# Kernel tuning notes

Hardware: AMD Instinct MI355X
Metric: run time of the kernel (lower is better)

The kernel has to match this reference:

```python
import jax, jax.numpy as jnp
import numpy as np

B, N, C, H, P = 8, 4096, 256, 4, 64  # batch, tokens, hidden, heads, proj_size


def setup_inputs() -> dict:
    key = jax.random.key(0)
    ks = jax.random.split(key, 6)
    sc = 0.02
    x = jax.random.normal(ks[0], (B, N, C), jnp.float32)
    bank = jax.random.normal(ks[1], (B, N, C), jnp.float32)  # unused by forward, kept for fidelity
    W_qkvv = jax.random.normal(ks[2], (4 * C, C), jnp.float32) * sc  # Linear(C, 4C), no bias
    W_E = jax.random.normal(ks[3], (P, N), jnp.float32) * sc          # E = F shared Linear(N, P)
    b_E = jnp.zeros((P,), jnp.float32)
    temperature = jnp.ones((H, 1, 1), jnp.float32)
    temperature2 = jnp.ones((H, 1, 1), jnp.float32)
    W_out1 = jax.random.normal(ks[4], (C // 2, C), jnp.float32) * sc  # out_proj (spatial branch)
    b_out1 = jnp.zeros((C // 2,), jnp.float32)
    W_out2 = jax.random.normal(ks[5], (C // 2, C), jnp.float32) * sc  # out_proj2 (channel branch)
    b_out2 = jnp.zeros((C // 2,), jnp.float32)
    prelu_a = jnp.array(0.25, jnp.float32)  # nn.PReLU() default: single shared slope
    return {"x": x, "bank": bank, "W_qkvv": W_qkvv, "W_E": W_E, "b_E": b_E,
            "temperature": temperature, "temperature2": temperature2,
            "W_out1": W_out1, "b_out1": b_out1, "W_out2": W_out2, "b_out2": b_out2,
            "prelu_a": prelu_a}


def _l2norm(t):
    # torch F.normalize(dim=-1): x / max(||x||_2, eps)
    return t / jnp.maximum(jnp.linalg.norm(t, axis=-1, keepdims=True), 1e-12)


def reference(x, bank, W_qkvv, W_E, b_E, temperature, temperature2,
              W_out1, b_out1, W_out2, b_out2, prelu_a):
    Bb, Nn, Cc = x.shape
    Hh = temperature.shape[0]
    d = Cc // Hh
    # qkvv projection -> [4, B, H, N, d], then transpose token/feature axes -> [B, H, d, N]
    qkvv = (x @ W_qkvv.T).reshape(Bb, Nn, 4, Hh, d).transpose(2, 0, 3, 1, 4)
    q, k, v_ca, v_sa = (qkvv[0].transpose(0, 1, 3, 2), qkvv[1].transpose(0, 1, 3, 2),
                        qkvv[2].transpose(0, 1, 3, 2), qkvv[3].transpose(0, 1, 3, 2))
    # shared linear E=F projects the token axis N -> P (applied to UNnormalized k, v_sa)
    k_proj = jnp.einsum('bhdn,pn->bhdp', k, W_E) + b_E      # [B,H,d,P]
    v_sa_proj = jnp.einsum('bhdn,pn->bhdp', v_sa, W_E) + b_E  # [B,H,d,P]
    qn = _l2norm(q)
    kn = _l2norm(k)
    # channel attention: [B,H,d,d]
    attn_ca = jax.nn.softmax(jnp.einsum('bhdn,bhen->bhde', qn, kn) * temperature, axis=-1)
    x_ca = jnp.einsum('bhde,bhen->bhdn', attn_ca, v_ca).transpose(0, 3, 1, 2).reshape(Bb, Nn, Cc)
    # spatial attention (projected): [B,H,N,P]
    attn_sa = jax.nn.softmax(jnp.einsum('bhdn,bhdp->bhnp', qn, k_proj) * temperature2, axis=-1)
    x_sa = jnp.einsum('bhnp,bhdp->bhnd', attn_sa, v_sa_proj).transpose(0, 2, 1, 3).reshape(Bb, Nn, Cc)
    x_sa = x_sa @ W_out1.T + b_out1
    x_ca = x_ca @ W_out2.T + b_out2
    out = jnp.concatenate([x_sa, x_ca], axis=-1)
    return jnp.where(out >= 0, out, prelu_a * out)  # PReLU
```

## Files before the change

kernel.cpp:

```cpp
#include <hip/hip_runtime.h>
#include <cstdint>
#include <cstddef>

constexpr int B_ = 8, N_ = 4096, C_ = 256, H_ = 4, D_ = 64, P_ = 64;
constexpr int OC_ = 4 * C_;
constexpr int M_  = B_ * N_;
constexpr int GX_ROWS = 320;
constexpr int KSPLIT_G = 8;

#define DEV_INLINE __device__ __forceinline__

typedef unsigned short ushort_t;
typedef __attribute__((ext_vector_type(8))) short short8;
typedef __attribute__((ext_vector_type(4))) short short4v;
typedef __attribute__((ext_vector_type(4))) float floatx4;

DEV_INLINE short f2bf(float f) {
  unsigned int u = __builtin_bit_cast(unsigned int, f);
  u += 0x7FFFu + ((u >> 16) & 1u);
  return (short)(u >> 16);
}
DEV_INLINE float bf2f(ushort_t u) {
  return __builtin_bit_cast(float, (unsigned int)u << 16);
}

constexpr size_t X4_  = (size_t)M_ * C_ / 4;
constexpr size_t WQ4_ = (size_t)OC_ * C_ / 4;
constexpr size_t W14_ = (size_t)128 * C_ / 4;
constexpr size_t WE4_ = (size_t)P_ * N_ / 4;
constexpr size_t TOT4_ = X4_ + WQ4_ + 2 * W14_ + WE4_;

__global__ __launch_bounds__(256) void k_cast(const float* __restrict__ x,
                                              const float* __restrict__ Wq,
                                              const float* __restrict__ W1,
                                              const float* __restrict__ W2,
                                              const float* __restrict__ WE,
                                              ushort_t* __restrict__ xb,
                                              ushort_t* __restrict__ wqb,
                                              ushort_t* __restrict__ w1b,
                                              ushort_t* __restrict__ w2b,
                                              ushort_t* __restrict__ web) {
  const size_t stride = (size_t)gridDim.x * 256;
  for (size_t i = blockIdx.x * 256 + threadIdx.x; i < TOT4_; i += stride) {
    const float* src;
    ushort_t* dst;
    size_t o;
    if (i < X4_) { src = x; dst = xb; o = i; }
    else if (i < X4_ + WQ4_) { src = Wq; dst = wqb; o = i - X4_; }
    else if (i < X4_ + WQ4_ + W14_) { src = W1; dst = w1b; o = i - X4_ - WQ4_; }
    else if (i < X4_ + WQ4_ + 2 * W14_) { src = W2; dst = w2b; o = i - X4_ - WQ4_ - W14_; }
    else { src = WE; dst = web; o = i - X4_ - WQ4_ - 2 * W14_; }
    float4 v = ((const float4*)src)[o];
    short4v s = {f2bf(v.x), f2bf(v.y), f2bf(v.z), f2bf(v.w)};
    *(short4v*)&dst[o * 4] = s;
  }
}

__global__ __launch_bounds__(256) void k_gram(const ushort_t* __restrict__ xb,
                                              const ushort_t* __restrict__ web,
                                              float* __restrict__ Gx) {
  __shared__ __align__(16) short As[128 * 64];
  __shared__ __align__(16) short Bs[128 * 64];
  const int job = blockIdx.x;
  const int ablk = job >> 1;
  const int bblk = job & 1;
  const int b = blockIdx.y >> 3;
  const int ksp = blockIdx.y & 7;
  const int t = threadIdx.x;
  const int lane = t & 63, wave = t >> 6;
  const int m16 = lane & 15, quad = lane >> 4;
  const int wm = (wave >> 1) << 6, wn = (wave & 1) << 6;
  floatx4 acc[4][4];
#pragma unroll
  for (int i = 0; i < 4; ++i)
#pragma unroll
    for (int j = 0; j < 4; ++j) acc[i][j] = (floatx4)(0.f);
  if (ablk == 2) {
#pragma unroll
    for (int i = 0; i < 8; ++i)
      *(unsigned int*)&As[64 * 64 + (i * 256 + t) * 2] = 0u;
  }
  const int c0 = (t & 31) * 4;
  const int tp = t >> 5;
#pragma unroll 1
  for (int it = 0; it < N_ / KSPLIT_G / 64; ++it) {
    const int n0 = ksp * (N_ / KSPLIT_G) + it * 64;
    __syncthreads();
#pragma unroll
    for (int q = 0; q < 4; ++q) {
      const int tok = q * 16 + 2 * tp;
      const size_t r0 = (size_t)(b * N_ + n0 + tok) * C_ + bblk * 128 + c0;
      short4v aa = *(const short4v*)&xb[r0];
      short4v cc = *(const short4v*)&xb[r0 + C_];
#pragma unroll
      for (int i = 0; i < 4; ++i) {
        const int r = c0 + i;
        const int col = tok ^ (8 * ((r >> 3) & 7));
        unsigned int w = (unsigned int)(ushort_t)aa[i] |
                         ((unsigned int)(ushort_t)cc[i] << 16);
        *(unsigned int*)&Bs[r * 64 + col] = w;
      }
    }
    if (ablk < 2) {
#pragma unroll
      for (int q = 0; q < 4; ++q) {
        const int tok = q * 16 + 2 * tp;
        const size_t r0 = (size_t)(b * N_ + n0 + tok) * C_ + ablk * 128 + c0;
        short4v aa = *(const short4v*)&xb[r0];
        short4v cc = *(const short4v*)&xb[r0 + C_];
#pragma unroll
        for (int i = 0; i < 4; ++i) {
          const int r = c0 + i;
          const int col = tok ^ (8 * ((r >> 3) & 7));
          unsigned int w = (unsigned int)(ushort_t)aa[i] |
                           ((unsigned int)(ushort_t)cc[i] << 16);
          *(unsigned int*)&As[r * 64 + col] = w;
        }
      }
    } else {
      const int oc8 = (t & 7) * 8;
      const int p0 = t >> 3;
#pragma unroll
      for (int q = 0; q < 2; ++q) {
        const int p = p0 + 32 * q;
        short8 v = *(const short8*)&web[(size_t)p * N_ + n0 + oc8];
        *(short8*)&As[p * 64 + (oc8 ^ (8 * ((p >> 3) & 7)))] = v;
      }
    }
    __syncthreads();
#pragma unroll
    for (int ks = 0; ks < 2; ++ks) {
      const int boct = ks * 32 + quad * 8;
      short8 af[4], bf[4];
#pragma unroll
      for (int i = 0; i < 4; ++i) {
        const int rA = wm + i * 16 + m16;
        af[i] = *(const short8*)&As[rA * 64 + (boct ^ (8 * ((rA >> 3) & 7)))];
      }
#pragma unroll
      for (int j = 0; j < 4; ++j) {
        const int rB = wn + j * 16 + m16;
        bf[j] = *(const short8*)&Bs[rB * 64 + (boct ^ (8 * ((rB >> 3) & 7)))];
      }
#pragma unroll
      for (int i = 0; i < 4; ++i)
#pragma unroll
        for (int j = 0; j < 4; ++j)
          acc[i][j] = __builtin_amdgcn_mfma_f32_16x16x32_bf16(af[i], bf[j], acc[i][j], 0, 0, 0);
    }
  }
#pragma unroll
  for (int i = 0; i < 4; ++i)
#pragma unroll
    for (int r = 0; r < 4; ++r) {
      const int rib = wm + i * 16 + quad * 4 + r;
      if (ablk == 2 && rib >= 64) continue;
      const size_t rowoff =
          ((size_t)b * GX_ROWS + ablk * 128 + rib) * 256 + bblk * 128 + wn;
#pragma unroll
      for (int j = 0; j < 4; ++j)
        atomicAdd(&Gx[rowoff + 16 * j + m16], acc[i][j][r]);
    }
}

__global__ __launch_bounds__(256) void k_gcast(const float* __restrict__ Gx,
                                               ushort_t* __restrict__ Gxb) {
  const int i = blockIdx.x * 256 + threadIdx.x;
  float4 v = ((const float4*)Gx)[i];
  short4v s = {f2bf(v.x), f2bf(v.y), f2bf(v.z), f2bf(v.w)};
  *(short4v*)&Gxb[i * 4] = s;
}

__global__ __launch_bounds__(256) void k_qv_mfma(const ushort_t* __restrict__ xb,
                                                 const ushort_t* __restrict__ wqb,
                                                 ushort_t* __restrict__ qv) {
  __shared__ __align__(16) short As[128 * 72];
  __shared__ __align__(16) short Bs[128 * 72];
  const int bm = blockIdx.x * 128;
  const int bo = blockIdx.y * 128;
  const int wrow_base = bo < 256 ? bo : bo + 256;
  const int t = threadIdx.x;
  const int oc = t & 7;
  const int rr = t >> 3;
  const int lane = t & 63, wave = t >> 6;
  const int m16 = lane & 15, quad = lane >> 4;
  const int wm = (wave >> 1) << 6, wn = (wave & 1) << 6;
  floatx4 acc[4][4];
#pragma unroll
  for (int i = 0; i < 4; ++i)
#pragma unroll
    for (int j = 0; j < 4; ++j) acc[i][j] = (floatx4)(0.f);
#pragma unroll 1
  for (int k0 = 0; k0 < 256; k0 += 64) {
    short8 a8[4], b8[4];
#pragma unroll
    for (int j = 0; j < 4; ++j) {
      const int r = rr + 32 * j;
      a8[j] = *(const short8*)&xb[(size_t)(bm + r) * 256 + k0 + 8 * oc];
      b8[j] = *(const short8*)&wqb[(size_t)(wrow_base + r) * 256 + k0 + 8 * oc];
    }
    __syncthreads();
#pragma unroll
    for (int j = 0; j < 4; ++j) {
      const int r = rr + 32 * j;
      *(short8*)&As[r * 72 + 8 * oc] = a8[j];
      *(short8*)&Bs[r * 72 + 8 * oc] = b8[j];
    }
    __syncthreads();
#pragma unroll
    for (int ks = 0; ks < 2; ++ks) {
      short8 af[4], bf[4];
#pragma unroll
      for (int i = 0; i < 4; ++i)
        af[i] = *(const short8*)&As[(wm + i * 16 + m16) * 72 + ks * 32 + quad * 8];
#pragma unroll
      for (int j = 0; j < 4; ++j)
        bf[j] = *(const short8*)&Bs[(wn + j * 16 + m16) * 72 + ks * 32 + quad * 8];
#pragma unroll
      for (int i = 0; i < 4; ++i)
#pragma unroll
        for (int j = 0; j < 4; ++j)
          acc[i][j] = __builtin_amdgcn_mfma_f32_16x16x32_bf16(af[i], bf[j], acc[i][j], 0, 0, 0);
    }
  }
#pragma unroll
  for (int i = 0; i < 4; ++i)
#pragma unroll
    for (int r = 0; r < 4; ++r) {
      const int gr = bm + wm + i * 16 + quad * 4 + r;
#pragma unroll
      for (int j = 0; j < 4; ++j)
        qv[(size_t)gr * 512 + bo + wn + j * 16 + m16] = (ushort_t)f2bf(acc[i][j][r]);
    }
}

__global__ __launch_bounds__(256) void k_t2gemm(const ushort_t* __restrict__ wqb,
                                                const ushort_t* __restrict__ Gxb,
                                                ushort_t* __restrict__ T2b) {
  __shared__ __align__(16) short As[128 * 72];
  __shared__ __align__(16) short Bs[128 * 72];
  const int bm = blockIdx.x * 128;
  const int b  = blockIdx.y >> 1;
  const int jb = blockIdx.y & 1;
  const int t = threadIdx.x;
  const int oc = t & 7;
  const int rr = t >> 3;
  const int lane = t & 63, wave = t >> 6;
  const int m16 = lane & 15, quad = lane >> 4;
  const int wm = (wave >> 1) << 6, wn = (wave & 1) << 6;
  const ushort_t* Bsrc = Gxb + ((size_t)b * GX_ROWS + jb * 128) * 256;
  floatx4 acc[4][4];
#pragma unroll
  for (int i = 0; i < 4; ++i)
#pragma unroll
    for (int j = 0; j < 4; ++j) acc[i][j] = (floatx4)(0.f);
#pragma unroll 1
  for (int k0 = 0; k0 < 256; k0 += 64) {
    short8 a8[4], b8[4];
#pragma unroll
    for (int j = 0; j < 4; ++j) {
      const int r = rr + 32 * j;
      a8[j] = *(const short8*)&wqb[(size_t)(bm + r) * 256 + k0 + 8 * oc];
      b8[j] = *(const short8*)&Bsrc[(size_t)r * 256 + k0 + 8 * oc];
    }
    __syncthreads();
#pragma unroll
    for (int j = 0; j < 4; ++j) {
      const int r = rr + 32 * j;
      *(short8*)&As[r * 72 + 8 * oc] = a8[j];
      *(short8*)&Bs[r * 72 + 8 * oc] = b8[j];
    }
    __syncthreads();
#pragma unroll
    for (int ks = 0; ks < 2; ++ks) {
      short8 af[4], bf[4];
#pragma unroll
      for (int i = 0; i < 4; ++i)
        af[i] = *(const short8*)&As[(wm + i * 16 + m16) * 72 + ks * 32 + quad * 8];
#pragma unroll
      for (int j = 0; j < 4; ++j)
        bf[j] = *(const short8*)&Bs[(wn + j * 16 + m16) * 72 + ks * 32 + quad * 8];
#pragma unroll
      for (int i = 0; i < 4; ++i)
#pragma unroll
        for (int j = 0; j < 4; ++j)
          acc[i][j] = __builtin_amdgcn_mfma_f32_16x16x32_bf16(af[i], bf[j], acc[i][j], 0, 0, 0);
    }
  }
#pragma unroll
  for (int i = 0; i < 4; ++i)
#pragma unroll
    for (int r = 0; r < 4; ++r) {
      const int gr = bm + wm + i * 16 + quad * 4 + r;
#pragma unroll
      for (int j = 0; j < 4; ++j)
        T2b[((size_t)b * 512 + gr) * 256 + jb * 128 + wn + j * 16 + m16] =
            (ushort_t)f2bf(acc[i][j][r]);
    }
}

__global__ __launch_bounds__(256) void k_rn(const ushort_t* __restrict__ wqb,
                                            const ushort_t* __restrict__ T2b,
                                            float* __restrict__ rn) {
  const int row_g = blockIdx.x * 4 + (threadIdx.x >> 6);
  const int lane = threadIdx.x & 63;
  const int b = row_g >> 9, row = row_g & 511;
  const short4v w  = *(const short4v*)&wqb[(size_t)row * 256 + lane * 4];
  const short4v tv = *(const short4v*)&T2b[((size_t)b * 512 + row) * 256 + lane * 4];
  float s = 0.f;
#pragma unroll
  for (int i = 0; i < 4; ++i) s += bf2f((ushort_t)w[i]) * bf2f((ushort_t)tv[i]);
#pragma unroll
  for (int o = 32; o; o >>= 1) s += __shfl_xor(s, o);
  if (lane == 0) rn[row_g] = 1.f / fmaxf(sqrtf(s), 1e-12f);
}

__global__ __launch_bounds__(64) void k_small(const ushort_t* __restrict__ wqb,
                                              const ushort_t* __restrict__ T2b,
                                              const ushort_t* __restrict__ Gxb,
                                              const float* __restrict__ bE,
                                              const float* __restrict__ rn,
                                              const float* __restrict__ t2,
                                              float* __restrict__ Sqk,
                                              ushort_t* __restrict__ ksb,
                                              ushort_t* __restrict__ vsb) {
  const int bh = blockIdx.x;
  const int job = blockIdx.y;
  const int b = bh >> 2, h = bh & 3;
  const int lane = threadIdx.x & 63;
  const int m16 = lane & 15, quad = lane >> 4;
  const int Abase = (job == 0 ? 0 : (job == 1 ? 256 : 768)) + h * 64;
  const ushort_t* Bp = (job == 0)
      ? T2b + ((size_t)b * 512 + 256 + h * 64) * 256
      : Gxb + ((size_t)b * GX_ROWS + 256) * 256;
  floatx4 acc[4][4];
#pragma unroll
  for (int i = 0; i < 4; ++i)
#pragma unroll
    for (int j = 0; j < 4; ++j) acc[i][j] = (floatx4)(0.f);
#pragma unroll
  for (int ks = 0; ks < 8; ++ks) {
    const int boct = ks * 32 + quad * 8;
    short8 af[4], bf[4];
#pragma unroll
    for (int i = 0; i < 4; ++i)
      af[i] = *(const short8*)&wqb[(size_t)(Abase + 16 * i + m16) * 256 + boct];
#pragma unroll
    for (int j = 0; j < 4; ++j)
      bf[j] = *(const short8*)&Bp[(size_t)(16 * j + m16) * 256 + boct];
#pragma unroll
    for (int i = 0; i < 4; ++i)
#pragma unroll
      for (int j = 0; j < 4; ++j)
        acc[i][j] = __builtin_amdgcn_mfma_f32_16x16x32_bf16(af[i], bf[j], acc[i][j], 0, 0, 0);
  }
  if (job == 0) {
#pragma unroll
    for (int i = 0; i < 4; ++i)
#pragma unroll
      for (int r = 0; r < 4; ++r) {
        const int d = 16 * i + quad * 4 + r;
#pragma unroll
        for (int j = 0; j < 4; ++j)
          Sqk[(size_t)bh * 4096 + d * 64 + 16 * j + m16] = acc[i][j][r];
      }
  } else if (job == 1) {
    const float tt = t2[h];
#pragma unroll
    for (int i = 0; i < 4; ++i)
#pragma unroll
      for (int r = 0; r < 4; ++r) {
        const int d = 16 * i + quad * 4 + r;
        const float rq = rn[b * 512 + h * 64 + d];
#pragma unroll
        for (int j = 0; j < 4; ++j) {
          const int p = 16 * j + m16;
          ksb[(size_t)bh * 4096 + p * 64 + d] =
              (ushort_t)f2bf((acc[i][j][r] + bE[p]) * rq * tt);
        }
      }
  } else {
#pragma unroll
    for (int i = 0; i < 4; ++i)
#pragma unroll
      for (int r = 0; r < 4; ++r) {
        const int d = 16 * i + quad * 4 + r;
#pragma unroll
        for (int j = 0; j < 4; ++j) {
          const int p = 16 * j + m16;
          vsb[(size_t)bh * 4096 + d * 64 + p] = (ushort_t)f2bf(acc[i][j][r] + bE[p]);
        }
      }
  }
}

__global__ __launch_bounds__(256) void k_ca_softmax(const float* __restrict__ Sqk,
                                                    const float* __restrict__ rn,
                                                    const float* __restrict__ temp,
                                                    ushort_t* __restrict__ ab) {
  const int w = threadIdx.x >> 6;
  const int lane = threadIdx.x & 63;
  const int row = blockIdx.x * 4 + w;
  const int b = row >> 8;
  const int rem = row & 255;
  const int h = rem >> 6;
  const float rq = rn[b * 512 + rem];
  const float rk = rn[b * 512 + 256 + h * 64 + lane];
  float l = Sqk[(size_t)row * 64 + lane] * rq * rk * temp[h];
  float m = l;
#pragma unroll
  for (int o = 32; o; o >>= 1) m = fmaxf(m, __shfl_xor(m, o));
  const float e = __expf(l - m);
  float s = e;
#pragma unroll
  for (int o = 32; o; o >>= 1) s += __shfl_xor(s, o);
  ab[(size_t)row * 64 + lane] = (ushort_t)f2bf(e / s);
}

__global__ __launch_bounds__(256) void k_ca_mfma(const ushort_t* __restrict__ qv,
                                                 const ushort_t* __restrict__ ab,
                                                 ushort_t* __restrict__ x_ca) {
  const int bh = blockIdx.x;
  const int b = bh >> 2, h = bh & 3;
  const int n0 = blockIdx.y * 128;
  const int lane = threadIdx.x & 63, wave = threadIdx.x >> 6;
  const int m16 = lane & 15, quad = lane >> 4;
  const ushort_t* abb = ab + (size_t)bh * 4096;
  short8 bf[2][4];
#pragma unroll
  for (int ks = 0; ks < 2; ++ks)
#pragma unroll
    for (int j = 0; j < 4; ++j)
      bf[ks][j] = *(const short8*)&abb[(16 * j + m16) * 64 + ks * 32 + quad * 8];
#pragma unroll
  for (int mm = 0; mm < 2; ++mm) {
    const int tokbase = n0 + 64 * mm + 16 * wave;
    const ushort_t* vrow =
        qv + (size_t)(b * N_ + tokbase + m16) * 512 + 256 + h * 64 + quad * 8;
    short8 af0 = *(const short8*)&vrow[0];
    short8 af1 = *(const short8*)&vrow[32];
    floatx4 o[4];
#pragma unroll
    for (int j = 0; j < 4; ++j) o[j] = (floatx4)(0.f);
#pragma unroll
    for (int j = 0; j < 4; ++j) {
      o[j] = __builtin_amdgcn_mfma_f32_16x16x32_bf16(af0, bf[0][j], o[j], 0, 0, 0);
      o[j] = __builtin_amdgcn_mfma_f32_16x16x32_bf16(af1, bf[1][j], o[j], 0, 0, 0);
    }
#pragma unroll
    for (int j = 0; j < 4; ++j)
#pragma unroll
      for (int r = 0; r < 4; ++r)
        x_ca[(size_t)(b * N_ + tokbase + quad * 4 + r) * C_ + h * 64 + 16 * j + m16] =
            (ushort_t)f2bf(o[j][r]);
  }
}

__global__ __launch_bounds__(256) void k_sa_mfma(const ushort_t* __restrict__ qv,
                                                 const ushort_t* __restrict__ ksb,
                                                 const ushort_t* __restrict__ vsb,
                                                 ushort_t* __restrict__ x_sa) {
  __shared__ float Pl[64][68];
  const int bh = blockIdx.x;
  const int b = bh >> 2, h = bh & 3;
  const int n0 = blockIdx.y * 64;
  const int lane = threadIdx.x & 63, wave = threadIdx.x >> 6;
  const int m16 = lane & 15, quad = lane >> 4;
  const ushort_t* qrow =
      qv + (size_t)(b * N_ + n0 + 16 * wave + m16) * 512 + h * 64 + quad * 8;
  short8 qf0 = *(const short8*)&qrow[0];
  short8 qf1 = *(const short8*)&qrow[32];
  const ushort_t* kb = ksb + (size_t)bh * 4096;
  const ushort_t* vb = vsb + (size_t)bh * 4096;
  short8 kf[2][4], vf[2][4];
#pragma unroll
  for (int ks = 0; ks < 2; ++ks)
#pragma unroll
    for (int j = 0; j < 4; ++j) {
      kf[ks][j] = *(const short8*)&kb[(16 * j + m16) * 64 + ks * 32 + quad * 8];
      vf[ks][j] = *(const short8*)&vb[(16 * j + m16) * 64 + ks * 32 + quad * 8];
    }
  floatx4 s[4];
#pragma unroll
  for (int j = 0; j < 4; ++j) s[j] = (floatx4)(0.f);
#pragma unroll
  for (int j = 0; j < 4; ++j) {
    s[j] = __builtin_amdgcn_mfma_f32_16x16x32_bf16(qf0, kf[0][j], s[j], 0, 0, 0);
    s[j] = __builtin_amdgcn_mfma_f32_16x16x32_bf16(qf1, kf[1][j], s[j], 0, 0, 0);
  }
  float p[4][4];
#pragma unroll
  for (int r = 0; r < 4; ++r) {
    float mr = fmaxf(fmaxf(s[0][r], s[1][r]), fmaxf(s[2][r], s[3][r]));
    mr = fmaxf(mr, __shfl_xor(mr, 1));
    mr = fmaxf(mr, __shfl_xor(mr, 2));
    mr = fmaxf(mr, __shfl_xor(mr, 4));
    mr = fmaxf(mr, __shfl_xor(mr, 8));
    float sr = 0.f;
#pragma unroll
    for (int j = 0; j < 4; ++j) {
      const float e = __expf(s[j][r] - mr);
      p[j][r] = e;
      sr += e;
    }
    sr += __shfl_xor(sr, 1);
    sr += __shfl_xor(sr, 2);
    sr += __shfl_xor(sr, 4);
    sr += __shfl_xor(sr, 8);
    const float inv = 1.f / sr;
#pragma unroll
    for (int j = 0; j < 4; ++j) p[j][r] *= inv;
  }
#pragma unroll
  for (int j = 0; j < 4; ++j)
#pragma unroll
    for (int r = 0; r < 4; ++r)
      Pl[16 * wave + quad * 4 + r][16 * j + m16] = p[j][r];
  __syncthreads();
  short8 pf[2];
#pragma unroll
// ... 67 lines not shown
#pragma unroll
    for (int ks = 0; ks < 2; ++ks) {
      short8 af[4], bf[4];
#pragma unroll
      for (int i = 0; i < 4; ++i)
        af[i] = *(const short8*)&As[(wm + i * 16 + m16) * 72 + ks * 32 + quad * 8];
#pragma unroll
      for (int j = 0; j < 4; ++j)
        bf[j] = *(const short8*)&Bs[(wn + j * 16 + m16) * 72 + ks * 32 + quad * 8];
#pragma unroll
      for (int i = 0; i < 4; ++i)
#pragma unroll
        for (int j = 0; j < 4; ++j)
          acc[i][j] = __builtin_amdgcn_mfma_f32_16x16x32_bf16(af[i], bf[j], acc[i][j], 0, 0, 0);
    }
  }
  const float slope = pa[0];
  float bj[4];
#pragma unroll
  for (int j = 0; j < 4; ++j) bj[j] = bias[wn + j * 16 + m16];
#pragma unroll
  for (int i = 0; i < 4; ++i)
#pragma unroll
    for (int r = 0; r < 4; ++r) {
      const int gr = bm + wm + i * 16 + quad * 4 + r;
#pragma unroll
      for (int j = 0; j < 4; ++j) {
        float v = acc[i][j][r] + bj[j];
        v = v >= 0.f ? v : slope * v;
        out[(size_t)gr * C_ + half * 128 + wn + j * 16 + m16] = v;
      }
    }
}

extern "C" void kernel_launch(void* const* d_in, const int* in_sizes, int n_in,
                              void* d_out, int out_size, void* d_ws, size_t ws_size,
                              hipStream_t stream) {
  (void)in_sizes; (void)n_in; (void)out_size; (void)ws_size;
  const float* x  = (const float*)d_in[0];
  const float* Wq = (const float*)d_in[2];
  const float* WE = (const float*)d_in[3];
  const float* bE = (const float*)d_in[4];
  const float* t1 = (const float*)d_in[5];
  const float* t2 = (const float*)d_in[6];
  const float* W1 = (const float*)d_in[7];
  const float* b1 = (const float*)d_in[8];
  const float* W2 = (const float*)d_in[9];
  const float* b2 = (const float*)d_in[10];
  const float* pa = (const float*)d_in[11];
  float* out = (float*)d_out;

  float* ws = (float*)d_ws;
  size_t off = 0;
  float* Sqk = ws + off; off += (size_t)32 * 4096;
  float* rn  = ws + off; off += (size_t)B_ * 512;
  float* Gx  = ws + off; off += (size_t)B_ * GX_ROWS * 256;
  ushort_t* qv  = (ushort_t*)(ws + off); off += (size_t)M_ * 512 / 2;
  ushort_t* xsa = (ushort_t*)(ws + off); off += (size_t)M_ * C_ / 2;
  ushort_t* xca = (ushort_t*)(ws + off); off += (size_t)M_ * C_ / 2;
  ushort_t* ksb = (ushort_t*)(ws + off); off += 32 * 4096 / 2;
  ushort_t* vsb = (ushort_t*)(ws + off); off += 32 * 4096 / 2;
  ushort_t* ab  = (ushort_t*)(ws + off); off += 32 * 4096 / 2;
  ushort_t* xb  = (ushort_t*)(ws + off); off += (size_t)M_ * C_ / 2;
  ushort_t* wqb = (ushort_t*)(ws + off); off += (size_t)OC_ * C_ / 2;
  ushort_t* w1b = (ushort_t*)(ws + off); off += (size_t)128 * C_ / 2;
  ushort_t* w2b = (ushort_t*)(ws + off); off += (size_t)128 * C_ / 2;
  ushort_t* web = (ushort_t*)(ws + off); off += (size_t)P_ * N_ / 2;
  ushort_t* Gxb = (ushort_t*)(ws + off); off += (size_t)B_ * GX_ROWS * 256 / 2;
  ushort_t* T2b = (ushort_t*)(ws + off); off += (size_t)B_ * 512 * 256 / 2;

  hipMemsetAsync(Gx, 0, (size_t)B_ * GX_ROWS * 256 * sizeof(float), stream);

  k_cast<<<2048, 256, 0, stream>>>(x, Wq, W1, W2, WE, xb, wqb, w1b, w2b, web);
  k_gram<<<dim3(6, B_ * KSPLIT_G), 256, 0, stream>>>(xb, web, Gx);
  k_qv_mfma<<<dim3(M_ / 128, 4), 256, 0, stream>>>(xb, wqb, qv);
  k_gcast<<<640, 256, 0, stream>>>(Gx, Gxb);
  k_t2gemm<<<dim3(4, B_ * 2), 256, 0, stream>>>(wqb, Gxb, T2b);
  k_rn<<<1024, 256, 0, stream>>>(wqb, T2b, rn);
  k_small<<<dim3(32, 3), 64, 0, stream>>>(wqb, T2b, Gxb, bE, rn, t2, Sqk, ksb, vsb);
  k_ca_softmax<<<512, 256, 0, stream>>>(Sqk, rn, t1, ab);
  k_ca_mfma<<<dim3(32, 32), 256, 0, stream>>>(qv, ab, xca);
  k_sa_mfma<<<dim3(32, 64), 256, 0, stream>>>(qv, ksb, vsb, xsa);
  k_out_mfma<<<dim3(M_ / 128, 2), 256, 0, stream>>>(xsa, xca, w1b, b1, w2b, b2, pa, out);
}
```

Baseline: 234.4 us.

## Fuse cast, QV GEMM, gram, norms and softmax into fewer kernel launches

Folds the fp32-to-bf16 cast of x into the QV projection GEMM, which now runs with 512-thread blocks and also writes xb. A side slice of that grid casts the weights. The gram kernel loads each x tile once for all column blocks and doubles the split-K factor. The separate Gx cast, norm and softmax kernels are folded into the mid kernels, and the channel and spatial attention kernels are merged into one launch. The aim is to cut kernel launches and intermediate global round-trips. In exchange, the fused kernels carry more branching and register pressure, and the larger split-K adds more atomics.

Result: slower. 255.8 us (+9.1%).

```diff
diff --git a/kernel.cpp b/kernel.cpp
--- a/kernel.cpp
+++ b/kernel.cpp
@@ -6,7 +6,7 @@
 constexpr int OC_ = 4 * C_;
 constexpr int M_  = B_ * N_;
 constexpr int GX_ROWS = 320;
-constexpr int KSPLIT_G = 8;
+constexpr int KSPLIT_G = 16;
 
 #define DEV_INLINE __device__ __forceinline__
 
@@ -23,220 +23,217 @@
 DEV_INLINE float bf2f(ushort_t u) {
   return __builtin_bit_cast(float, (unsigned int)u << 16);
 }
-
-constexpr size_t X4_  = (size_t)M_ * C_ / 4;
-constexpr size_t WQ4_ = (size_t)OC_ * C_ / 4;
-constexpr size_t W14_ = (size_t)128 * C_ / 4;
-constexpr size_t WE4_ = (size_t)P_ * N_ / 4;
-constexpr size_t TOT4_ = X4_ + WQ4_ + 2 * W14_ + WE4_;
-
-__global__ __launch_bounds__(256) void k_cast(const float* __restrict__ x,
-                                              const float* __restrict__ Wq,
-                                              const float* __restrict__ W1,
-                                              const float* __restrict__ W2,
-                                              const float* __restrict__ WE,
-                                              ushort_t* __restrict__ xb,
-                                              ushort_t* __restrict__ wqb,
-                                              ushort_t* __restrict__ w1b,
-                                              ushort_t* __restrict__ w2b,
-                                              ushort_t* __restrict__ web) {
-  const size_t stride = (size_t)gridDim.x * 256;
-  for (size_t i = blockIdx.x * 256 + threadIdx.x; i < TOT4_; i += stride) {
-    const float* src;
-    ushort_t* dst;
-    size_t o;
-    if (i < X4_) { src = x; dst = xb; o = i; }
-    else if (i < X4_ + WQ4_) { src = Wq; dst = wqb; o = i - X4_; }
-    else if (i < X4_ + WQ4_ + W14_) { src = W1; dst = w1b; o = i - X4_ - WQ4_; }
-    else if (i < X4_ + WQ4_ + 2 * W14_) { src = W2; dst = w2b; o = i - X4_ - WQ4_ - W14_; }
-    else { src = WE; dst = web; o = i - X4_ - WQ4_ - 2 * W14_; }
-    float4 v = ((const float4*)src)[o];
-    short4v s = {f2bf(v.x), f2bf(v.y), f2bf(v.z), f2bf(v.w)};
-    *(short4v*)&dst[o * 4] = s;
-  }
-}
-
-__global__ __launch_bounds__(256) void k_gram(const ushort_t* __restrict__ xb,
+DEV_INLINE short4v cvt4(float4 v) {
+  short4v s = {f2bf(v.x), f2bf(v.y), f2bf(v.z), f2bf(v.w)};
+  return s;
+}
+
+__global__ __launch_bounds__(512) void k_qv(const float* __restrict__ x,
+                                            const float* __restrict__ Wq,
+                                            const float* __restrict__ WE,
+                                            const float* __restrict__ W1,
+                                            const float* __restrict__ W2,
+                                            ushort_t* __restrict__ xb,
+                                            ushort_t* __restrict__ wqb,
+                                            ushort_t* __restrict__ web,
+                                            ushort_t* __restrict__ w1b,
+                                            ushort_t* __restrict__ w2b,
+                                            ushort_t* __restrict__ qv) {
+  __shared__ __align__(16) short As[128 * 72];
+  __shared__ __align__(16) short Bs[256 * 72];
+  const int cs = blockIdx.y;
+  const int t = threadIdx.x;
+  if (cs == 2) {
+    constexpr size_t WQ4 = 65536, WE4 = 65536, W14 = 8192;
+    constexpr size_t TOTW4 = WQ4 + WE4 + 2 * W14;
+    for (size_t i = (size_t)blockIdx.x * 512 + t; i < TOTW4; i += (size_t)256 * 512) {
+      const float* src; ushort_t* dst; size_t o;
+      if (i < WQ4) { src = Wq; dst = wqb; o = i; }
+      else if (i < WQ4 + WE4) { src = WE; dst = web; o = i - WQ4; }
+      else if (i < WQ4 + WE4 + W14) { src = W1; dst = w1b; o = i - WQ4 - WE4; }
+      else { src = W2; dst = w2b; o = i - WQ4 - WE4 - W14; }
+      float4 v = ((const float4*)src)[o];
+      *(short4v*)&dst[o * 4] = cvt4(v);
+    }
+    return;
+  }
+  const int bm = blockIdx.x * 128;
+  const int wbase = cs ? 512 : 0;
+  const int c = (t & 15) * 4;
+  const int row = t >> 4;
+  const int lane = t & 63, wave = t >> 6;
+  const int m16 = lane & 15, quad = lane >> 4;
+  const int wm = (wave >> 2) << 6, wn = (wave & 3) << 6;
+  floatx4 acc[4][4];
+#pragma unroll
+  for (int i = 0; i < 4; ++i)
+#pragma unroll
+    for (int j = 0; j < 4; ++j) acc[i][j] = (floatx4)(0.f);
+#pragma unroll 1
+  for (int k0 = 0; k0 < 256; k0 += 64) {
+    float4 av[4], bv[8];
+#pragma unroll
+    for (int rep = 0; rep < 4; ++rep)
+      av[rep] = *(const float4*)&x[(size_t)(bm + row + 32 * rep) * 256 + k0 + c];
+#pragma unroll
+    for (int rep = 0; rep < 8; ++rep)
+      bv[rep] = *(const float4*)&Wq[(size_t)(wbase + row + 32 * rep) * 256 + k0 + c];
+    __syncthreads();
+#pragma unroll
+    for (int rep = 0; rep < 4; ++rep) {
+      short4v s = cvt4(av[rep]);
+      *(short4v*)&As[(row + 32 * rep) * 72 + c] = s;
+      if (cs == 0)
+        *(short4v*)&xb[(size_t)(bm + row + 32 * rep) * 256 + k0 + c] = s;
+    }
+#pragma unroll
+    for (int rep = 0; rep < 8; ++rep)
+      *(short4v*)&Bs[(row + 32 * rep) * 72 + c] = cvt4(bv[rep]);
+    __syncthreads();
+#pragma unroll
+    for (int ks = 0; ks < 2; ++ks) {
+      short8 af[4], bf[4];
+#pragma unroll
+      for (int i = 0; i < 4; ++i)
+        af[i] = *(const short8*)&As[(wm + i * 16 + m16) * 72 + ks * 32 + quad * 8];
+#pragma unroll
+      for (int j = 0; j < 4; ++j)
+        bf[j] = *(const short8*)&Bs[(wn + j * 16 + m16) * 72 + ks * 32 + quad * 8];
+#pragma unroll
+      for (int i = 0; i < 4; ++i)
+#pragma unroll
+        for (int j = 0; j < 4; ++j)
+          acc[i][j] = __builtin_amdgcn_mfma_f32_16x16x32_bf16(af[i], bf[j], acc[i][j], 0, 0, 0);
+    }
+  }
+#pragma unroll
+  for (int i = 0; i < 4; ++i)
+#pragma unroll
+    for (int r = 0; r < 4; ++r) {
+      const int gr = bm + wm + i * 16 + quad * 4 + r;
+#pragma unroll
+      for (int j = 0; j < 4; ++j)
+        qv[(size_t)gr * 512 + cs * 256 + wn + j * 16 + m16] =
+            (ushort_t)f2bf(acc[i][j][r]);
+    }
+}
+
+__global__ __launch_bounds__(512) void k_gram(const ushort_t* __restrict__ xb,
                                               const ushort_t* __restrict__ web,
                                               float* __restrict__ Gx) {
-  __shared__ __align__(16) short As[128 * 64];
-  __shared__ __align__(16) short Bs[128 * 64];
+  __shared__ __align__(16) short Bs[256 * 64];
+  __shared__ __align__(16) short Ws[64 * 64];
   const int job = blockIdx.x;
-  const int ablk = job >> 1;
-  const int bblk = job & 1;
-  const int b = blockIdx.y >> 3;
-  const int ksp = blockIdx.y & 7;
+  const int b = blockIdx.y >> 4;
+  const int ksp = blockIdx.y & 15;
   const int t = threadIdx.x;
   const int lane = t & 63, wave = t >> 6;
   const int m16 = lane & 15, quad = lane >> 4;
-  const int wm = (wave >> 1) << 6, wn = (wave & 1) << 6;
+  const int wm = (wave >> 2) << 6;
+  const int wn4 = (wave & 3) << 6;
+  const int wn2 = wave << 5;
+  const int c0 = (t & 63) * 4;
+  const int tp = t >> 6;
   floatx4 acc[4][4];
 #pragma unroll
   for (int i = 0; i < 4; ++i)
 #pragma unroll
     for (int j = 0; j < 4; ++j) acc[i][j] = (floatx4)(0.f);
-  if (ablk == 2) {
-#pragma unroll
-    for (int i = 0; i < 8; ++i)
-      *(unsigned int*)&As[64 * 64 + (i * 256 + t) * 2] = 0u;
-  }
-  const int c0 = (t & 31) * 4;
-  const int tp = t >> 5;
 #pragma unroll 1
-  for (int it = 0; it < N_ / KSPLIT_G / 64; ++it) {
+  for (int it = 0; it < 4; ++it) {
     const int n0 = ksp * (N_ / KSPLIT_G) + it * 64;
     __syncthreads();
 #pragma unroll
     for (int q = 0; q < 4; ++q) {
       const int tok = q * 16 + 2 * tp;
-      const size_t r0 = (size_t)(b * N_ + n0 + tok) * C_ + bblk * 128 + c0;
+      const size_t r0 = (size_t)(b * N_ + n0 + tok) * C_ + c0;
       short4v aa = *(const short4v*)&xb[r0];
       short4v cc = *(const short4v*)&xb[r0 + C_];
 #pragma unroll
-      for (int i = 0; i < 4; ++i) {
-        const int r = c0 + i;
+      for (int ii = 0; ii < 4; ++ii) {
+        const int r = c0 + ii;
         const int col = tok ^ (8 * ((r >> 3) & 7));
-        unsigned int w = (unsigned int)(ushort_t)aa[i] |
-                         ((unsigned int)(ushort_t)cc[i] << 16);
+        unsigned int w = (unsigned int)(ushort_t)aa[ii] |
+                         ((unsigned int)(ushort_t)cc[ii] << 16);
         *(unsigned int*)&Bs[r * 64 + col] = w;
       }
     }
-    if (ablk < 2) {
-#pragma unroll
-      for (int q = 0; q < 4; ++q) {
-        const int tok = q * 16 + 2 * tp;
-        const size_t r0 = (size_t)(b * N_ + n0 + tok) * C_ + ablk * 128 + c0;
-        short4v aa = *(const short4v*)&xb[r0];
-        short4v cc = *(const short4v*)&xb[r0 + C_];
-#pragma unroll
-        for (int i = 0; i < 4; ++i) {
-          const int r = c0 + i;
-          const int col = tok ^ (8 * ((r >> 3) & 7));
-          unsigned int w = (unsigned int)(ushort_t)aa[i] |
-                           ((unsigned int)(ushort_t)cc[i] << 16);
-          *(unsigned int*)&As[r * 64 + col] = w;
-        }
-      }
-    } else {
+    if (job == 2) {
       const int oc8 = (t & 7) * 8;
       const int p0 = t >> 3;
-#pragma unroll
-      for (int q = 0; q < 2; ++q) {
-        const int p = p0 + 32 * q;
-        short8 v = *(const short8*)&web[(size_t)p * N_ + n0 + oc8];
-        *(short8*)&As[p * 64 + (oc8 ^ (8 * ((p >> 3) & 7)))] = v;
-      }
+      short8 v = *(const short8*)&web[(size_t)p0 * N_ + n0 + oc8];
+      *(short8*)&Ws[p0 * 64 + (oc8 ^ (8 * ((p0 >> 3) & 7)))] = v;
     }
     __syncthreads();
 #pragma unroll
     for (int ks = 0; ks < 2; ++ks) {
       const int boct = ks * 32 + quad * 8;
-      short8 af[4], bf[4];
-#pragma unroll
-      for (int i = 0; i < 4; ++i) {
-        const int rA = wm + i * 16 + m16;
-        af[i] = *(const short8*)&As[rA * 64 + (boct ^ (8 * ((rA >> 3) & 7)))];
-      }
-#pragma unroll
-      for (int j = 0; j < 4; ++j) {
-        const int rB = wn + j * 16 + m16;
-        bf[j] = *(const short8*)&Bs[rB * 64 + (boct ^ (8 * ((rB >> 3) & 7)))];
-      }
-#pragma unroll
-      for (int i = 0; i < 4; ++i)
+      if (job < 2) {
+        short8 af[4], bf[4];
+#pragma unroll
+        for (int i = 0; i < 4; ++i) {
+          const int rA = job * 128 + wm + 16 * i + m16;
+          af[i] = *(const short8*)&Bs[rA * 64 + (boct ^ (8 * ((rA >> 3) & 7)))];
+        }
+#pragma unroll
+        for (int j = 0; j < 4; ++j) {
+          const int rB = wn4 + 16 * j + m16;
+          bf[j] = *(const short8*)&Bs[rB * 64 + (boct ^ (8 * ((rB >> 3) & 7)))];
+        }
+#pragma unroll
+        for (int i = 0; i < 4; ++i)
+#pragma unroll
+          for (int j = 0; j < 4; ++j)
+            acc[i][j] = __builtin_amdgcn_mfma_f32_16x16x32_bf16(af[i], bf[j], acc[i][j], 0, 0, 0);
+      } else {
+        short8 af[4], bf[2];
+#pragma unroll
+        for (int i = 0; i < 4; ++i) {
+          const int rA = 16 * i + m16;
+          af[i] = *(const short8*)&Ws[rA * 64 + (boct ^ (8 * ((rA >> 3) & 7)))];
+        }
+#pragma unroll
+        for (int j = 0; j < 2; ++j) {
+          const int rB = wn2 + 16 * j + m16;
+          bf[j] = *(const short8*)&Bs[rB * 64 + (boct ^ (8 * ((rB >> 3) & 7)))];
+        }
+#pragma unroll
+        for (int i = 0; i < 4; ++i)
+#pragma unroll
+          for (int j = 0; j < 2; ++j)
+            acc[i][j] = __builtin_amdgcn_mfma_f32_16x16x32_bf16(af[i], bf[j], acc[i][j], 0, 0, 0);
+      }
+    }
+  }
+  if (job < 2) {
+#pragma unroll
+    for (int i = 0; i < 4; ++i)
+#pragma unroll
+      for (int r = 0; r < 4; ++r) {
+        const int grow = job * 128 + wm + 16 * i + quad * 4 + r;
+        const size_t rowoff = ((size_t)b * GX_ROWS + grow) * 256;
 #pragma unroll
         for (int j = 0; j < 4; ++j)
-          acc[i][j] = __builtin_amdgcn_mfma_f32_16x16x32_bf16(af[i], bf[j], acc[i][j], 0, 0, 0);
-    }
-  }
-#pragma unroll
-  for (int i = 0; i < 4; ++i)
-#pragma unroll
-    for (int r = 0; r < 4; ++r) {
-      const int rib = wm + i * 16 + quad * 4 + r;
-      if (ablk == 2 && rib >= 64) continue;
-      const size_t rowoff =
-          ((size_t)b * GX_ROWS + ablk * 128 + rib) * 256 + bblk * 128 + wn;
-#pragma unroll
-      for (int j = 0; j < 4; ++j)
-        atomicAdd(&Gx[rowoff + 16 * j + m16], acc[i][j][r]);
-    }
-}
-
-__global__ __launch_bounds__(256) void k_gcast(const float* __restrict__ Gx,
-                                               ushort_t* __restrict__ Gxb) {
-  const int i = blockIdx.x * 256 + threadIdx.x;
-  float4 v = ((const float4*)Gx)[i];
-  short4v s = {f2bf(v.x), f2bf(v.y), f2bf(v.z), f2bf(v.w)};
-  *(short4v*)&Gxb[i * 4] = s;
-}
-
-__global__ __launch_bounds__(256) void k_qv_mfma(const ushort_t* __restrict__ xb,
-                                                 const ushort_t* __restrict__ wqb,
-                                                 ushort_t* __restrict__ qv) {
-  __shared__ __align__(16) short As[128 * 72];
-  __shared__ __align__(16) short Bs[128 * 72];
-  const int bm = blockIdx.x * 128;
-  const int bo = blockIdx.y * 128;
-  const int wrow_base = bo < 256 ? bo : bo + 256;
-  const int t = threadIdx.x;
-  const int oc = t & 7;
-  const int rr = t >> 3;
-  const int lane = t & 63, wave = t >> 6;
-  const int m16 = lane & 15, quad = lane >> 4;
-  const int wm = (wave >> 1) << 6, wn = (wave & 1) << 6;
-  floatx4 acc[4][4];
-#pragma unroll
-  for (int i = 0; i < 4; ++i)
-#pragma unroll
-    for (int j = 0; j < 4; ++j) acc[i][j] = (floatx4)(0.f);
-#pragma unroll 1
-  for (int k0 = 0; k0 < 256; k0 += 64) {
-    short8 a8[4], b8[4];
-#pragma unroll
-    for (int j = 0; j < 4; ++j) {
-      const int r = rr + 32 * j;
-      a8[j] = *(const short8*)&xb[(size_t)(bm + r) * 256 + k0 + 8 * oc];
-      b8[j] = *(const short8*)&wqb[(size_t)(wrow_base + r) * 256 + k0 + 8 * oc];
-    }
-    __syncthreads();
-#pragma unroll
-    for (int j = 0; j < 4; ++j) {
-      const int r = rr + 32 * j;
-      *(short8*)&As[r * 72 + 8 * oc] = a8[j];
-      *(short8*)&Bs[r * 72 + 8 * oc] = b8[j];
-    }
-    __syncthreads();
-#pragma unroll
-    for (int ks = 0; ks < 2; ++ks) {
-      short8 af[4], bf[4];
-#pragma unroll
-      for (int i = 0; i < 4; ++i)
-        af[i] = *(const short8*)&As[(wm + i * 16 + m16) * 72 + ks * 32 + quad * 8];
-#pragma unroll
-      for (int j = 0; j < 4; ++j)
-        bf[j] = *(const short8*)&Bs[(wn + j * 16 + m16) * 72 + ks * 32 + quad * 8];
-#pragma unroll
-      for (int i = 0; i < 4; ++i)
-#pragma unroll
-        for (int j = 0; j < 4; ++j)
-          acc[i][j] = __builtin_amdgcn_mfma_f32_16x16x32_bf16(af[i], bf[j], acc[i][j], 0, 0, 0);
-    }
-  }
-#pragma unroll
-  for (int i = 0; i < 4; ++i)
-#pragma unroll
-    for (int r = 0; r < 4; ++r) {
-      const int gr = bm + wm + i * 16 + quad * 4 + r;
-#pragma unroll
-      for (int j = 0; j < 4; ++j)
-        qv[(size_t)gr * 512 + bo + wn + j * 16 + m16] = (ushort_t)f2bf(acc[i][j][r]);
-    }
-}
-
-__global__ __launch_bounds__(256) void k_t2gemm(const ushort_t* __restrict__ wqb,
-                                                const ushort_t* __restrict__ Gxb,
-                                                ushort_t* __restrict__ T2b) {
+          atomicAdd(&Gx[rowoff + wn4 + 16 * j + m16], acc[i][j][r]);
+      }
+  } else {
+#pragma unroll
+    for (int i = 0; i < 4; ++i)
+#pragma unroll
+      for (int r = 0; r < 4; ++r) {
+        const int grow = 256 + 16 * i + quad * 4 + r;
+        const size_t rowoff = ((size_t)b * GX_ROWS + grow) * 256;
+#pragma unroll
+        for (int j = 0; j < 2; ++j)
+          atomicAdd(&Gx[rowoff + wn2 + 16 * j + m16], acc[i][j][r]);
+      }
+  }
+}
+
+__global__ __launch_bounds__(256) void k_mid1(const ushort_t* __restrict__ wqb,
+                                              const float* __restrict__ Gx,
+                                              ushort_t* __restrict__ T2b,
+                                              float* __restrict__ ssq) {
   __shared__ __align__(16) short As[128 * 72];
   __shared__ __align__(16) short Bs[128 * 72];
   const int bm = blockIdx.x * 128;
@@ -248,7 +245,7 @@
   const int lane = t & 63, wave = t >> 6;
   const int m16 = lane & 15, quad = lane >> 4;
   const int wm = (wave >> 1) << 6, wn = (wave & 1) << 6;
-  const ushort_t* Bsrc = Gxb + ((size_t)b * GX_ROWS + jb * 128) * 256;
+  const float* Bsrc = Gx + ((size_t)b * GX_ROWS + jb * 128) * 256;
   floatx4 acc[4][4];
 #pragma unroll
   for (int i = 0; i < 4; ++i)
@@ -261,7 +258,12 @@
     for (int j = 0; j < 4; ++j) {
       const int r = rr + 32 * j;
       a8[j] = *(const short8*)&wqb[(size_t)(bm + r) * 256 + k0 + 8 * oc];
-      b8[j] = *(const short8*)&Bsrc[(size_t)r * 256 + k0 + 8 * oc];
+      float4 g0 = *(const float4*)&Bsrc[(size_t)r * 256 + k0 + 8 * oc];
+      float4 g1 = *(const float4*)&Bsrc[(size_t)r * 256 + k0 + 8 * oc + 4];
+      short8 bb;
+      bb[0] = f2bf(g0.x); bb[1] = f2bf(g0.y); bb[2] = f2bf(g0.z); bb[3] = f2bf(g0.w);
+      bb[4] = f2bf(g1.x); bb[5] = f2bf(g1.y); bb[6] = f2bf(g1.z); bb[7] = f2bf(g1.w);
+      b8[j] = bb;
     }
     __syncthreads();
 #pragma unroll
@@ -292,47 +294,37 @@
 #pragma unroll
     for (int r = 0; r < 4; ++r) {
       const int gr = bm + wm + i * 16 + quad * 4 + r;
-#pragma unroll
-      for (int j = 0; j < 4; ++j)
-        T2b[((size_t)b * 512 + gr) * 256 + jb * 128 + wn + j * 16 + m16] =
-            (ushort_t)f2bf(acc[i][j][r]);
-    }
-}
-
-__global__ __launch_bounds__(256) void k_rn(const ushort_t* __restrict__ wqb,
-                                            const ushort_t* __restrict__ T2b,
-                                            float* __restrict__ rn) {
-  const int row_g = blockIdx.x * 4 + (threadIdx.x >> 6);
-  const int lane = threadIdx.x & 63;
-  const int b = row_g >> 9, row = row_g & 511;
-  const short4v w  = *(const short4v*)&wqb[(size_t)row * 256 + lane * 4];
-  const short4v tv = *(const short4v*)&T2b[((size_t)b * 512 + row) * 256 + lane * 4];
-  float s = 0.f;
-#pragma unroll
-  for (int i = 0; i < 4; ++i) s += bf2f((ushort_t)w[i]) * bf2f((ushort_t)tv[i]);
-#pragma unroll
-  for (int o = 32; o; o >>= 1) s += __shfl_xor(s, o);
-  if (lane == 0) rn[row_g] = 1.f / fmaxf(sqrtf(s), 1e-12f);
-}
-
-__global__ __launch_bounds__(64) void k_small(const ushort_t* __restrict__ wqb,
-                                              const ushort_t* __restrict__ T2b,
-                                              const ushort_t* __restrict__ Gxb,
-                                              const float* __restrict__ bE,
-                                              const float* __restrict__ rn,
-                                              const float* __restrict__ t2,
-                                              float* __restrict__ Sqk,
-                                              ushort_t* __restrict__ ksb,
-                                              ushort_t* __restrict__ vsb) {
+      float s = 0.f;
+#pragma unroll
+      for (int j = 0; j < 4; ++j) {
+        const int col = jb * 128 + wn + j * 16 + m16;
+        T2b[((size_t)b * 512 + gr) * 256 + col] = (ushort_t)f2bf(acc[i][j][r]);
+        s += bf2f(wqb[(size_t)gr * 256 + col]) * acc[i][j][r];
+      }
+      s += __shfl_xor(s, 1);
+      s += __shfl_xor(s, 2);
+      s += __shfl_xor(s, 4);
+      s += __shfl_xor(s, 8);
+      if (m16 == 0) atomicAdd(&ssq[b * 512 + gr], s);
+    }
+}
+
+__global__ __launch_bounds__(64) void k_mid2(const ushort_t* __restrict__ wqb,
+                                             const ushort_t* __restrict__ T2b,
+                                             const float* __restrict__ Gx,
+                                             const float* __restrict__ ssq,
+                                             const float* __restrict__ bE,
+                                             const float* __restrict__ t1,
+                                             const float* __restrict__ t2,
+                                             ushort_t* __restrict__ ab,
+                                             ushort_t* __restrict__ ksb,
+                                             ushort_t* __restrict__ vsb) {
   const int bh = blockIdx.x;
   const int job = blockIdx.y;
   const int b = bh >> 2, h = bh & 3;
   const int lane = threadIdx.x & 63;
   const int m16 = lane & 15, quad = lane >> 4;
   const int Abase = (job == 0 ? 0 : (job == 1 ? 256 : 768)) + h * 64;
-  const ushort_t* Bp = (job == 0)
-      ? T2b + ((size_t)b * 512 + 256 + h * 64) * 256
-      : Gxb + ((size_t)b * GX_ROWS + 256) * 256;
   floatx4 acc[4][4];
 #pragma unroll
   for (int i = 0; i < 4; ++i)
@@ -345,24 +337,65 @@
 #pragma unroll
     for (int i = 0; i < 4; ++i)
       af[i] = *(const short8*)&wqb[(size_t)(Abase + 16 * i + m16) * 256 + boct];
+    if (job == 0) {
+#pragma unroll
+      for (int j = 0; j < 4; ++j)
+        bf[j] = *(const short8*)&T2b[((size_t)b * 512 + 256 + h * 64 + 16 * j + m16) * 256 + boct];
+    } else {
+#pragma unroll
+      for (int j = 0; j < 4; ++j) {
+        const float* gp = Gx + ((size_t)b * GX_ROWS + 256 + 16 * j + m16) * 256 + boct;
+        float4 g0 = *(const float4*)gp;
+        float4 g1 = *(const float4*)(gp + 4);
+        short8 bb;
+        bb[0] = f2bf(g0.x); bb[1] = f2bf(g0.y); bb[2] = f2bf(g0.z); bb[3] = f2bf(g0.w);
+        bb[4] = f2bf(g1.x); bb[5] = f2bf(g1.y); bb[6] = f2bf(g1.z); bb[7] = f2bf(g1.w);
+        bf[j] = bb;
+      }
+    }
+#pragma unroll
+    for (int i = 0; i < 4; ++i)
+#pragma unroll
+      for (int j = 0; j < 4; ++j)
+        acc[i][j] = __builtin_amdgcn_mfma_f32_16x16x32_bf16(af[i], bf[j], acc[i][j], 0, 0, 0);
+  }
+  if (job == 0) {
+    const float t1h = t1[h];
+    float rnk[4];
 #pragma unroll
     for (int j = 0; j < 4; ++j)
-      bf[j] = *(const short8*)&Bp[(size_t)(16 * j + m16) * 256 + boct];
-#pragma unroll
-    for (int i = 0; i < 4; ++i)
-#pragma unroll
-      for (int j = 0; j < 4; ++j)
-        acc[i][j] = __builtin_amdgcn_mfma_f32_16x16x32_bf16(af[i], bf[j], acc[i][j], 0, 0, 0);
-  }
-  if (job == 0) {
+      rnk[j] = 1.f / fmaxf(sqrtf(ssq[b * 512 + 256 + h * 64 + 16 * j + m16]), 1e-12f);
 #pragma unroll
     for (int i = 0; i < 4; ++i)
 #pragma unroll
       for (int r = 0; r < 4; ++r) {
         const int d = 16 * i + quad * 4 + r;
+        const float rq = 1.f / fmaxf(sqrtf(ssq[b * 512 + h * 64 + d]), 1e-12f);
+        float l[4];
+        float m = -1e30f;
+#pragma unroll
+        for (int j = 0; j < 4; ++j) {
+          l[j] = acc[i][j][r] * rq * rnk[j] * t1h;
+          m = fmaxf(m, l[j]);
+        }
+        m = fmaxf(m, __shfl_xor(m, 1));
+        m = fmaxf(m, __shfl_xor(m, 2));
+        m = fmaxf(m, __shfl_xor(m, 4));
+        m = fmaxf(m, __shfl_xor(m, 8));
+        float s = 0.f;
+#pragma unroll
+        for (int j = 0; j < 4; ++j) {
+          l[j] = __expf(l[j] - m);
+          s += l[j];
+        }
+        s += __shfl_xor(s, 1);
+        s += __shfl_xor(s, 2);
+        s += __shfl_xor(s, 4);
+        s += __shfl_xor(s, 8);
+        const float inv = 1.f / s;
 #pragma unroll
         for (int j = 0; j < 4; ++j)
-          Sqk[(size_t)bh * 4096 + d * 64 + 16 * j + m16] = acc[i][j][r];
+          ab[(size_t)bh * 4096 + d * 64 + 16 * j + m16] = (ushort_t)f2bf(l[j] * inv);
       }
   } else if (job == 1) {
     const float tt = t2[h];
@@ -371,7 +404,7 @@
 #pragma unroll
       for (int r = 0; r < 4; ++r) {
         const int d = 16 * i + quad * 4 + r;
-        const float rq = rn[b * 512 + h * 64 + d];
+        const float rq = 1.f / fmaxf(sqrtf(ssq[b * 512 + h * 64 + d]), 1e-12f);
 #pragma unroll
         for (int j = 0; j < 4; ++j) {
           const int p = 16 * j + m16;
@@ -394,78 +427,51 @@
   }
 }
 
-__global__ __launch_bounds__(256) void k_ca_softmax(const float* __restrict__ Sqk,
-                                                    const float* __restrict__ rn,
-                                                    const float* __restrict__ temp,
-                                                    ushort_t* __restrict__ ab) {
-  const int w = threadIdx.x >> 6;
-  const int lane = threadIdx.x & 63;
-  const int row = blockIdx.x * 4 + w;
-  const int b = row >> 8;
-  const int rem = row & 255;
-  const int h = rem >> 6;
-  const float rq = rn[b * 512 + rem];
-  const float rk = rn[b * 512 + 256 + h * 64 + lane];
-  float l = Sqk[(size_t)row * 64 + lane] * rq * rk * temp[h];
-  float m = l;
-#pragma unroll
-  for (int o = 32; o; o >>= 1) m = fmaxf(m, __shfl_xor(m, o));
-  const float e = __expf(l - m);
-  float s = e;
-#pragma unroll
-  for (int o = 32; o; o >>= 1) s += __shfl_xor(s, o);
-  ab[(size_t)row * 64 + lane] = (ushort_t)f2bf(e / s);
-}
-
-__global__ __launch_bounds__(256) void k_ca_mfma(const ushort_t* __restrict__ qv,
-                                                 const ushort_t* __restrict__ ab,
-                                                 ushort_t* __restrict__ x_ca) {
-  const int bh = blockIdx.x;
-  const int b = bh >> 2, h = bh & 3;
-  const int n0 = blockIdx.y * 128;
-  const int lane = threadIdx.x & 63, wave = threadIdx.x >> 6;
-  const int m16 = lane & 15, quad = lane >> 4;
-  const ushort_t* abb = ab + (size_t)bh * 4096;
-  short8 bf[2][4];
-#pragma unroll
-  for (int ks = 0; ks < 2; ++ks)
-#pragma unroll
-    for (int j = 0; j < 4; ++j)
-      bf[ks][j] = *(const short8*)&abb[(16 * j + m16) * 64 + ks * 32 + quad * 8];
-#pragma unroll
-  for (int mm = 0; mm < 2; ++mm) {
-    const int tokbase = n0 + 64 * mm + 16 * wave;
-    const ushort_t* vrow =
-        qv + (size_t)(b * N_ + tokbase + m16) * 512 + 256 + h * 64 + quad * 8;
-    short8 af0 = *(const short8*)&vrow[0];
-    short8 af1 = *(const short8*)&vrow[32];
-    floatx4 o[4];
-#pragma unroll
-    for (int j = 0; j < 4; ++j) o[j] = (floatx4)(0.f);
-#pragma unroll
-    for (int j = 0; j < 4; ++j) {
-      o[j] = __builtin_amdgcn_mfma_f32_16x16x32_bf16(af0, bf[0][j], o[j], 0, 0, 0);
-      o[j] = __builtin_amdgcn_mfma_f32_16x16x32_bf16(af1, bf[1][j], o[j], 0, 0, 0);
-    }
-#pragma unroll
-    for (int j = 0; j < 4; ++j)
-#pragma unroll
-      for (int r = 0; r < 4; ++r)
-        x_ca[(size_t)(b * N_ + tokbase + quad * 4 + r) * C_ + h * 64 + 16 * j + m16] =
-            (ushort_t)f2bf(o[j][r]);
-  }
-}
-
-__global__ __launch_bounds__(256) void k_sa_mfma(const ushort_t* __restrict__ qv,
-                                                 const ushort_t* __restrict__ ksb,
-                                                 const ushort_t* __restrict__ vsb,
-                                                 ushort_t* __restrict__ x_sa) {
+__global__ __launch_bounds__(256) void k_attn(const ushort_t* __restrict__ qv,
+                                              const ushort_t* __restrict__ ab,
+                                              const ushort_t* __restrict__ ksb,
+                                              const ushort_t* __restrict__ vsb,
+                                              ushort_t* __restrict__ x_ca,
+                                              ushort_t* __restrict__ x_sa) {
   __shared__ float Pl[64][68];
   const int bh = blockIdx.x;
   const int b = bh >> 2, h = bh & 3;
-  const int n0 = blockIdx.y * 64;
   const int lane = threadIdx.x & 63, wave = threadIdx.x >> 6;
   const int m16 = lane & 15, quad = lane >> 4;
+  if (blockIdx.y < 32) {
+    const int n0 = blockIdx.y * 128;
+    const ushort_t* abb = ab + (size_t)bh * 4096;
+    short8 bf[2][4];
+#pragma unroll
+    for (int ks = 0; ks < 2; ++ks)
+#pragma unroll
+      for (int j = 0; j < 4; ++j)
+        bf[ks][j] = *(const short8*)&abb[(16 * j + m16) * 64 + ks * 32 + quad * 8];
+#pragma unroll
+    for (int mm = 0; mm < 2; ++mm) {
+      const int tokbase = n0 + 64 * mm + 16 * wave;
+      const ushort_t* vrow =
+          qv + (size_t)(b * N_ + tokbase + m16) * 512 + 256 + h * 64 + quad * 8;
+      short8 af0 = *(const short8*)&vrow[0];
+      short8 af1 = *(const short8*)&vrow[32];
+      floatx4 o[4];
+#pragma unroll
+      for (int j = 0; j < 4; ++j) o[j] = (floatx4)(0.f);
+#pragma unroll
+      for (int j = 0; j < 4; ++j) {
+        o[j] = __builtin_amdgcn_mfma_f32_16x16x32_bf16(af0, bf[0][j], o[j], 0, 0, 0);
+        o[j] = __builtin_amdgcn_mfma_f32_16x16x32_bf16(af1, bf[1][j], o[j], 0, 0, 0);
+      }
+#pragma unroll
+      for (int j = 0; j < 4; ++j)
+#pragma unroll
+        for (int r = 0; r < 4; ++r)
+          x_ca[(size_t)(b * N_ + tokbase + quad * 4 + r) * C_ + h * 64 + 16 * j + m16] =
+              (ushort_t)f2bf(o[j][r]);
+    }
+    return;
+  }
+  const int n0 = (blockIdx.y - 32) * 64;
   const ushort_t* qrow =
       qv + (size_t)(b * N_ + n0 + 16 * wave + m16) * 512 + h * 64 + quad * 8;
   short8 qf0 = *(const short8*)&qrow[0];
@@ -639,9 +645,8 @@
 
   float* ws = (float*)d_ws;
   size_t off = 0;
-  float* Sqk = ws + off; off += (size_t)32 * 4096;
-  float* rn  = ws + off; off += (size_t)B_ * 512;
   float* Gx  = ws + off; off += (size_t)B_ * GX_ROWS * 256;
+  float* ssq = ws + off; off += (size_t)B_ * 512;
   ushort_t* qv  = (ushort_t*)(ws + off); off += (size_t)M_ * 512 / 2;
   ushort_t* xsa = (ushort_t*)(ws + off); off += (size_t)M_ * C_ / 2;
   ushort_t* xca = (ushort_t*)(ws + off); off += (size_t)M_ * C_ / 2;
@@ -653,20 +658,15 @@
   ushort_t* w1b = (ushort_t*)(ws + off); off += (size_t)128 * C_ / 2;
   ushort_t* w2b = (ushort_t*)(ws + off); off += (size_t)128 * C_ / 2;
   ushort_t* web = (ushort_t*)(ws + off); off += (size_t)P_ * N_ / 2;
-  ushort_t* Gxb = (ushort_t*)(ws + off); off += (size_t)B_ * GX_ROWS * 256 / 2;
-  ushort_t* T2b = (ushort_t*)(ws + off); off += (size_t)B_ * 512 * 256 / 2;
-
-  hipMemsetAsync(Gx, 0, (size_t)B_ * GX_ROWS * 256 * sizeof(float), stream);
-
-  k_cast<<<2048, 256, 0, stream>>>(x, Wq, W1, W2, WE, xb, wqb, w1b, w2b, web);
-  k_gram<<<dim3(6, B_ * KSPLIT_G), 256, 0, stream>>>(xb, web, Gx);
-  k_qv_mfma<<<dim3(M_ / 128, 4), 256, 0, stream>>>(xb, wqb, qv);
-  k_gcast<<<640, 256, 0, stream>>>(Gx, Gxb);
-  k_t2gemm<<<dim3(4, B_ * 2), 256, 0, stream>>>(wqb, Gxb, T2b);
-  k_rn<<<1024, 256, 0, stream>>>(wqb, T2b, rn);
-  k_small<<<dim3(32, 3), 64, 0, stream>>>(wqb, T2b, Gxb, bE, rn, t2, Sqk, ksb, vsb);
-  k_ca_softmax<<<512, 256, 0, stream>>>(Sqk, rn, t1, ab);
-  k_ca_mfma<<<dim3(32, 32), 256, 0, stream>>>(qv, ab, xca);
-  k_sa_mfma<<<dim3(32, 64), 256, 0, stream>>>(qv, ksb, vsb, xsa);
+  ushort_t* T2b = (ushort_t*)(ws + off); off += (size_t)B_ * 512 * C_ / 2;
+
+  hipMemsetAsync(Gx, 0, ((size_t)B_ * GX_ROWS * 256 + B_ * 512) * sizeof(float), stream);
+
+  k_qv<<<dim3(M_ / 128, 3), 512, 0, stream>>>(x, Wq, WE, W1, W2,
+                                              xb, wqb, web, w1b, w2b, qv);
+  k_gram<<<dim3(3, B_ * KSPLIT_G), 512, 0, stream>>>(xb, web, Gx);
+  k_mid1<<<dim3(4, B_ * 2), 256, 0, stream>>>(wqb, Gx, T2b, ssq);
+  k_mid2<<<dim3(32, 3), 64, 0, stream>>>(wqb, T2b, Gx, ssq, bE, t1, t2, ab, ksb, vsb);
+  k_attn<<<dim3(32, 96), 256, 0, stream>>>(qv, ab, ksb, vsb, xca, xsa);
   k_out_mfma<<<dim3(M_ / 128, 2), 256, 0, stream>>>(xsa, xca, w1b, b1, w2b, b2, pa, out);
 }
```
